# Optimization experiments

Hardware: AMD Instinct MI355X
Metric: run time of the kernel (lower is better)

The kernel has to match this reference:

```python
import jax, jax.numpy as jnp
import numpy as np

N_NODES = 50000   # batch_size * n_verts
N_EDGES = 800000
D_FEAT = 128
UNITS = 256


def setup_inputs() -> dict:
    key = jax.random.key(0)
    k1, k2, k3, k4, k5 = jax.random.split(key, 5)
    features = jax.random.normal(k1, (N_NODES, D_FEAT), dtype=jnp.float32)
    edge_row = jax.random.randint(k2, (N_EDGES,), 0, N_NODES, dtype=jnp.int32)
    edge_col = jax.random.randint(k3, (N_EDGES,), 0, N_NODES, dtype=jnp.int32)
    edge_val = jax.random.uniform(k4, (N_EDGES,), dtype=jnp.float32)
    W = jax.random.normal(k5, (D_FEAT, UNITS), dtype=jnp.float32) * (1.0 / np.sqrt(D_FEAT))
    return {"features": features, "edge_row": edge_row, "edge_col": edge_col,
            "edge_val": edge_val, "W": W}


def reference(features, edge_row, edge_col, edge_val, W):
    # features: [N, F] (already the (batch*n_verts, F) layout the layer reshapes to)
    # A in COO: A[edge_row[e], edge_col[e]] = edge_val[e]
    n = features.shape[0]
    # in_degree = row-sum of A values, +1 for self loop
    in_degree = jax.ops.segment_sum(edge_val, edge_row, num_segments=n) + 1.0
    invsqrt_deg = jax.lax.rsqrt(in_degree)                       # [N]
    normalized = invsqrt_deg[:, None] * features                 # [N, F]
    # pooled = A @ normalized  (gather source rows, scale, scatter-add to dest)
    msgs = edge_val[:, None] * normalized[edge_col]              # [E, F]
    pooled = jax.ops.segment_sum(msgs, edge_row, num_segments=n) # [N, F]
    # self-loop contribution (normalized case)
    pooled = pooled + invsqrt_deg[:, None] * normalized
    # dense projection + relu
    out = jax.nn.relu(pooled @ W)                                # [N, units]
    return out
```

## Files before the change

### kernel.cpp

```cpp
#include <hip/hip_runtime.h>

constexpr int N = 50000;
constexpr int E = 800000;
constexpr int F = 128;
constexpr int U = 256;

constexpr int R    = 4;
constexpr int NK   = N * R;
constexpr int EBLK = E / 256;
constexpr int SBLK = (NK + 255) / 256;

typedef __attribute__((ext_vector_type(8))) short short8;
typedef __attribute__((ext_vector_type(4))) float float4v;

constexpr float FIXED_SCALE = 67108864.0f;
constexpr float FIXED_INV   = 1.4901161193847656e-8f;
constexpr unsigned long long VAL_MASK = 0xFFFFFFFFFFull;

__device__ inline unsigned short f32_to_bf16(float x) {
    unsigned int u = __float_as_uint(x);
    unsigned int r = (u + 0x7fffu + ((u >> 16) & 1u)) >> 16;
    return (unsigned short)r;
}
__device__ inline float bf_lo(unsigned int u) { return __uint_as_float(u << 16); }
__device__ inline float bf_hi(unsigned int u) { return __uint_as_float(u & 0xffff0000u); }

__global__ __launch_bounds__(256) void hist_kernel(const int* __restrict__ erow,
                                                   const float* __restrict__ eval,
                                                   unsigned long long* __restrict__ packed,
                                                   unsigned int* __restrict__ rankp,
                                                   const float* __restrict__ W,
                                                   unsigned short* __restrict__ Wt) {
    if (blockIdx.x >= EBLK) {
        int idx = (blockIdx.x - EBLK) * 256 + threadIdx.x;
        int k = idx >> 8;
        int n = idx & 255;
        Wt[n * F + k] = f32_to_bf16(W[idx]);
        return;
    }
    int e = blockIdx.x * 256 + threadIdx.x;
    int key = erow[e] * R + (blockIdx.x & (R - 1));
    unsigned long long add =
        (1ull << 40) | (unsigned long long)(eval[e] * FIXED_SCALE);
    unsigned long long old = atomicAdd(&packed[key], add);
    rankp[e] = ((unsigned int)key << 12) | (unsigned int)(old >> 40);
}

__global__ __launch_bounds__(256) void blksum_kernel(const unsigned long long* __restrict__ packed,
                                                     int* __restrict__ blk_sum) {
    int i = blockIdx.x * 256 + threadIdx.x;
    int v = (i < NK) ? (int)(packed[i] >> 40) : 0;
    #pragma unroll
    for (int off = 32; off > 0; off >>= 1) v += __shfl_down(v, off, 64);
    __shared__ int s[4];
    if ((threadIdx.x & 63) == 0) s[threadIdx.x >> 6] = v;
    __syncthreads();
    if (threadIdx.x == 0) blk_sum[blockIdx.x] = s[0] + s[1] + s[2] + s[3];
}

__global__ __launch_bounds__(256) void blkscan_kernel(const unsigned long long* __restrict__ packed,
                                                      const int* __restrict__ blk_sum,
                                                      int* __restrict__ rp2) {
    __shared__ int sh[256];
    __shared__ int waves[4];
    __shared__ int base_sh;
    int t = threadIdx.x;
    int bid = blockIdx.x;

    int pre = 0;
    for (int idx = t; idx < bid; idx += 256) pre += blk_sum[idx];
    #pragma unroll
    for (int off = 32; off > 0; off >>= 1) pre += __shfl_down(pre, off, 64);
    if ((t & 63) == 0) waves[t >> 6] = pre;
    __syncthreads();
    if (t == 0) base_sh = waves[0] + waves[1] + waves[2] + waves[3];

    int i = bid * 256 + t;
    int v = (i < NK) ? (int)(packed[i] >> 40) : 0;
    sh[t] = v;
    __syncthreads();
    for (int off = 1; off < 256; off <<= 1) {
        int u = (t >= off) ? sh[t - off] : 0;
        __syncthreads();
        sh[t] += u;
        __syncthreads();
    }
    if (i < NK) rp2[i] = base_sh + sh[t] - v;
    if (bid == 0 && t == 0) rp2[NK] = E;
}

__global__ __launch_bounds__(256) void permute_kernel(const int* __restrict__ ecol,
                                                      const float* __restrict__ eval,
                                                      const unsigned int* __restrict__ rankp,
                                                      const int* __restrict__ rp2,
                                                      int2* __restrict__ csr) {
    int e = blockIdx.x * 256 + threadIdx.x;
    if (e < E) {
        unsigned int pk = rankp[e];
        int p = rp2[pk >> 12] + (int)(pk & 0xFFFu);
        csr[p] = make_int2(ecol[e], __float_as_int(eval[e]));
    }
}

__global__ __launch_bounds__(256) void norm_kernel(const float* __restrict__ feat,
                                                   const unsigned long long* __restrict__ packed,
                                                   float* __restrict__ iv,
                                                   unsigned int* __restrict__ nrm) {
    int gtid = blockIdx.x * 256 + threadIdx.x;
    int n    = gtid >> 6;
    int lane = threadIdx.x & 63;
    if (n >= N) return;

    int kb = n * R;
    unsigned long long s = (packed[kb] & VAL_MASK) + (packed[kb + 1] & VAL_MASK) +
                           (packed[kb + 2] & VAL_MASK) + (packed[kb + 3] & VAL_MASK);
    float iv_ = rsqrtf((float)s * FIXED_INV + 1.0f);
    if (lane == 0) iv[n] = iv_;

    float2 f = ((const float2*)feat)[n * 64 + lane];
    nrm[n * 64 + lane] =
        (unsigned int)f32_to_bf16(iv_ * f.x) | ((unsigned int)f32_to_bf16(iv_ * f.y) << 16);
}

__global__ __launch_bounds__(256) void gather_kernel(const int* __restrict__ rp2,
                                                     const int2* __restrict__ csr,
                                                     const unsigned int* __restrict__ nrm,
                                                     const float* __restrict__ iv,
                                                     unsigned int* __restrict__ pooledb) {
    int gtid = blockIdx.x * 256 + threadIdx.x;
    int n    = gtid >> 6;
    int lane = threadIdx.x & 63;
    if (n >= N) return;

    float iv_ = iv[n];
    unsigned int self = nrm[n * 64 + lane];
    float acc0 = iv_ * bf_lo(self);
    float acc1 = iv_ * bf_hi(self);

    int e = rp2[n * R], e1 = rp2[n * R + R];
    for (; e + 7 < e1; e += 8) {
        int2 p0 = csr[e],     p1 = csr[e + 1], p2 = csr[e + 2], p3 = csr[e + 3];
        int2 p4 = csr[e + 4], p5 = csr[e + 5], p6 = csr[e + 6], p7 = csr[e + 7];
        unsigned int u0 = nrm[(size_t)p0.x * 64 + lane];
        unsigned int u1 = nrm[(size_t)p1.x * 64 + lane];
        unsigned int u2 = nrm[(size_t)p2.x * 64 + lane];
        unsigned int u3 = nrm[(size_t)p3.x * 64 + lane];
        unsigned int u4 = nrm[(size_t)p4.x * 64 + lane];
        unsigned int u5 = nrm[(size_t)p5.x * 64 + lane];
        unsigned int u6 = nrm[(size_t)p6.x * 64 + lane];
        unsigned int u7 = nrm[(size_t)p7.x * 64 + lane];
        acc0 += __int_as_float(p0.y) * bf_lo(u0); acc1 += __int_as_float(p0.y) * bf_hi(u0);
        acc0 += __int_as_float(p1.y) * bf_lo(u1); acc1 += __int_as_float(p1.y) * bf_hi(u1);
        acc0 += __int_as_float(p2.y) * bf_lo(u2); acc1 += __int_as_float(p2.y) * bf_hi(u2);
        acc0 += __int_as_float(p3.y) * bf_lo(u3); acc1 += __int_as_float(p3.y) * bf_hi(u3);
        acc0 += __int_as_float(p4.y) * bf_lo(u4); acc1 += __int_as_float(p4.y) * bf_hi(u4);
        acc0 += __int_as_float(p5.y) * bf_lo(u5); acc1 += __int_as_float(p5.y) * bf_hi(u5);
        acc0 += __int_as_float(p6.y) * bf_lo(u6); acc1 += __int_as_float(p6.y) * bf_hi(u6);
        acc0 += __int_as_float(p7.y) * bf_lo(u7); acc1 += __int_as_float(p7.y) * bf_hi(u7);
    }
    for (; e + 3 < e1; e += 4) {
        int2 p0 = csr[e], p1 = csr[e + 1], p2 = csr[e + 2], p3 = csr[e + 3];
        unsigned int u0 = nrm[(size_t)p0.x * 64 + lane];
        unsigned int u1 = nrm[(size_t)p1.x * 64 + lane];
        unsigned int u2 = nrm[(size_t)p2.x * 64 + lane];
        unsigned int u3 = nrm[(size_t)p3.x * 64 + lane];
        acc0 += __int_as_float(p0.y) * bf_lo(u0); acc1 += __int_as_float(p0.y) * bf_hi(u0);
        acc0 += __int_as_float(p1.y) * bf_lo(u1); acc1 += __int_as_float(p1.y) * bf_hi(u1);
        acc0 += __int_as_float(p2.y) * bf_lo(u2); acc1 += __int_as_float(p2.y) * bf_hi(u2);
        acc0 += __int_as_float(p3.y) * bf_lo(u3); acc1 += __int_as_float(p3.y) * bf_hi(u3);
    }
    for (; e < e1; ++e) {
        int2 p0 = csr[e];
        unsigned int u0 = nrm[(size_t)p0.x * 64 + lane];
        acc0 += __int_as_float(p0.y) * bf_lo(u0);
        acc1 += __int_as_float(p0.y) * bf_hi(u0);
    }
    pooledb[n * 64 + lane] =
        (unsigned int)f32_to_bf16(acc0) | ((unsigned int)f32_to_bf16(acc1) << 16);
}

__global__ __launch_bounds__(256) void gemm_mfma_kernel(const unsigned short* __restrict__ Ab,
                                                        const unsigned short* __restrict__ Wt,
                                                        float* __restrict__ out) {
    __shared__ unsigned short As[16384];
    __shared__ unsigned short Bs[16384];
    const int tid = threadIdx.x;
    const int m0 = blockIdx.x * 128;
    const int n0 = blockIdx.y * 128;

    {
        const int r = tid >> 1;
        const int h = tid & 1;
        const int grow = m0 + r;
        const uint4* asrc = (grow < N) ? (const uint4*)(Ab + (size_t)grow * F) : nullptr;
        const uint4* bsrc = (const uint4*)(Wt + (size_t)(n0 + r) * F);
        #pragma unroll
        for (int j = 0; j < 8; ++j) {
            int o = h * 8 + j;
            int ks = o >> 2, quad = o & 3;
            int slot = ((ks * 8 + (r >> 4)) * 64) + (quad << 4) + (r & 15);
            uint4 av = asrc ? asrc[o] : make_uint4(0u, 0u, 0u, 0u);
            ((uint4*)As)[slot] = av;
            ((uint4*)Bs)[slot] = bsrc[o];
        }
    }
    __syncthreads();

    const int wave = tid >> 6;
    const int lane = tid & 63;
    float4v acc[8][2];
    #pragma unroll
    for (int i = 0; i < 8; ++i) {
        acc[i][0] = (float4v){0.f, 0.f, 0.f, 0.f};
        acc[i][1] = (float4v){0.f, 0.f, 0.f, 0.f};
    }

    #pragma unroll
    for (int ks = 0; ks < 4; ++ks) {
        short8 b0 = *(const short8*)&Bs[(((ks * 8 + wave * 2 + 0) * 64) + lane) * 8];
        short8 b1 = *(const short8*)&Bs[(((ks * 8 + wave * 2 + 1) * 64) + lane) * 8];
        #pragma unroll
        for (int mt = 0; mt < 8; ++mt) {
            short8 a = *(const short8*)&As[(((ks * 8 + mt) * 64) + lane) * 8];
            acc[mt][0] = __builtin_amdgcn_mfma_f32_16x16x32_bf16(a, b0, acc[mt][0], 0, 0, 0);
            acc[mt][1] = __builtin_amdgcn_mfma_f32_16x16x32_bf16(a, b1, acc[mt][1], 0, 0, 0);
        }
    }

    const int quad = lane >> 4;
    const int colt = lane & 15;
    #pragma unroll
    for (int mt = 0; mt < 8; ++mt) {
        #pragma unroll
        for (int nt = 0; nt < 2; ++nt) {
            int col = n0 + (wave * 2 + nt) * 16 + colt;
            #pragma unroll
            for (int i = 0; i < 4; ++i) {
                int row = m0 + mt * 16 + quad * 4 + i;
                if (row < N) out[(size_t)row * U + col] = fmaxf(acc[mt][nt][i], 0.f);
            }
        }
    }
}

extern "C" void kernel_launch(void* const* d_in, const int* in_sizes, int n_in,
                              void* d_out, int out_size, void* d_ws, size_t ws_size,
                              hipStream_t stream) {
    (void)in_sizes; (void)n_in; (void)out_size; (void)ws_size;

    const float* feat = (const float*)d_in[0];
    const int*   erow = (const int*)d_in[1];
    const int*   ecol = (const int*)d_in[2];
    const float* eval = (const float*)d_in[3];
    const float* W    = (const float*)d_in[4];
    float* out = (float*)d_out;

    char* ws = (char*)d_ws;
    unsigned long long* packed = (unsigned long long*)(ws + 0);
    int*            blk_sum = (int*)(ws + 1600000);
    int*            rp2     = (int*)(ws + 1603200);
    unsigned int*   rankp   = (unsigned int*)(ws + 2403264);
    int2*           csr     = (int2*)(ws + 5603264);
    float*          iv      = (float*)(ws + 12003264);
    unsigned short* Wt      = (unsigned short*)(ws + 12203264);
    unsigned int*   nrm     = (unsigned int*)(ws + 12268800);
    unsigned int*   pooledb = (unsigned int*)(ws + 25068800);

    (void)hipMemsetAsync(packed, 0, (size_t)NK * 8, stream);

    hist_kernel<<<EBLK + (F * U) / 256, 256, 0, stream>>>(erow, eval, packed, rankp, W, Wt);

    blksum_kernel<<<SBLK, 256, 0, stream>>>(packed, blk_sum);
    blkscan_kernel<<<SBLK, 256, 0, stream>>>(packed, blk_sum, rp2);

    permute_kernel<<<EBLK, 256, 0, stream>>>(ecol, eval, rankp, rp2, csr);
    norm_kernel  <<<(N * 64) / 256, 256, 0, stream>>>(feat, packed, iv, nrm);
    gather_kernel<<<(N * 64) / 256, 256, 0, stream>>>(rp2, csr, nrm, iv, pooledb);

    dim3 ggrid((N + 127) / 128, U / 128);
    gemm_mfma_kernel<<<ggrid, 256, 0, stream>>>((const unsigned short*)pooledb, Wt, out);
}
```

Measured before the change: 220.0 us.

## Fuse CSR-build front stages into one cooperative kernel with grid syncs

Replaces the memset, histogram, block-sum, block-scan, permute and normalize launches with a single cooperative kernel of 1024 blocks that uses grid-wide syncs between phases, with a multi-launch fallback. It also doubles the atomic spreading factor R from 4 to 8 to reduce atomic contention on row counters. The aim is to remove launch gaps and tail effects. In exchange, the scan pass now processes twice as many keys, the blkscan prefix loop over blk_sum grows, and grid syncs add their own cost.

```diff
diff --git a/kernel.cpp b/kernel.cpp
--- a/kernel.cpp
+++ b/kernel.cpp
@@ -1,11 +1,14 @@
 #include <hip/hip_runtime.h>
+#include <hip/hip_cooperative_groups.h>
+
+namespace cg = cooperative_groups;
 
 constexpr int N = 50000;
 constexpr int E = 800000;
 constexpr int F = 128;
 constexpr int U = 256;
 
-constexpr int R    = 4;
+constexpr int R    = 8;
 constexpr int NK   = N * R;
 constexpr int EBLK = E / 256;
 constexpr int SBLK = (NK + 255) / 256;
@@ -24,6 +27,121 @@
 }
 __device__ inline float bf_lo(unsigned int u) { return __uint_as_float(u << 16); }
 __device__ inline float bf_hi(unsigned int u) { return __uint_as_float(u & 0xffff0000u); }
+
+__device__ inline void p_zero(unsigned long long* packed, int g0, int gsz) {
+    for (int i = g0; i < NK; i += gsz) packed[i] = 0ull;
+}
+
+__device__ inline void p_hist(const int* erow, const float* eval,
+                              unsigned long long* packed, unsigned int* rankp,
+                              const float* W, unsigned short* Wt, int g0, int gsz) {
+    for (int e = g0; e < E; e += gsz) {
+        int key = erow[e] * R + ((e >> 8) & (R - 1));
+        unsigned long long add =
+            (1ull << 40) | (unsigned long long)(eval[e] * FIXED_SCALE);
+        unsigned long long old = atomicAdd(&packed[key], add);
+        rankp[e] = ((unsigned int)key << 12) | (unsigned int)(old >> 40);
+    }
+    for (int idx = g0; idx < F * U; idx += gsz) {
+        int k = idx >> 8, n = idx & 255;
+        Wt[n * F + k] = f32_to_bf16(W[idx]);
+    }
+}
+
+__device__ inline void p_blksum(const unsigned long long* packed, int* blk_sum,
+                                int bid0, int bstride, int t) {
+    __shared__ int s4[4];
+    for (int c = bid0; c < SBLK; c += bstride) {
+        int i = c * 256 + t;
+        int v = (i < NK) ? (int)(packed[i] >> 40) : 0;
+        #pragma unroll
+        for (int off = 32; off > 0; off >>= 1) v += __shfl_down(v, off, 64);
+        if ((t & 63) == 0) s4[t >> 6] = v;
+        __syncthreads();
+        if (t == 0) blk_sum[c] = s4[0] + s4[1] + s4[2] + s4[3];
+        __syncthreads();
+    }
+}
+
+__device__ inline void p_blkscan(const unsigned long long* packed, const int* blk_sum,
+                                 int* rp2, int bid0, int bstride, int t, int g0) {
+    __shared__ int sh[256];
+    __shared__ int waves[4];
+    __shared__ int base_sh;
+    for (int c = bid0; c < SBLK; c += bstride) {
+        int pre = 0;
+        for (int idx = t; idx < c; idx += 256) pre += blk_sum[idx];
+        #pragma unroll
+        for (int off = 32; off > 0; off >>= 1) pre += __shfl_down(pre, off, 64);
+        if ((t & 63) == 0) waves[t >> 6] = pre;
+        __syncthreads();
+        if (t == 0) base_sh = waves[0] + waves[1] + waves[2] + waves[3];
+        int i = c * 256 + t;
+        int v = (i < NK) ? (int)(packed[i] >> 40) : 0;
+        sh[t] = v;
+        __syncthreads();
+        for (int off = 1; off < 256; off <<= 1) {
+            int u = (t >= off) ? sh[t - off] : 0;
+            __syncthreads();
+            sh[t] += u;
+            __syncthreads();
+        }
+        if (i < NK) rp2[i] = base_sh + sh[t] - v;
+        __syncthreads();
+    }
+    if (g0 == 0) rp2[NK] = E;
+}
+
+__device__ inline void p_permute_norm(const int* ecol, const float* eval,
+                                      const unsigned int* rankp, const int* rp2,
+                                      int2* csr, const unsigned long long* packed,
+                                      const float* feat, float* iv, unsigned int* nrm,
+                                      int g0, int gsz, int t) {
+    for (int e = g0; e < E; e += gsz) {
+        unsigned int pk = rankp[e];
+        int p = rp2[pk >> 12] + (int)(pk & 0xFFFu);
+        csr[p] = make_int2(ecol[e], __float_as_int(eval[e]));
+    }
+    int lane = t & 63;
+    int w0 = g0 >> 6;
+    int wstride = gsz >> 6;
+    for (int n = w0; n < N; n += wstride) {
+        int kb = n * R;
+        unsigned long long s = 0;
+        #pragma unroll
+        for (int j = 0; j < R; ++j) s += packed[kb + j] & VAL_MASK;
+        float iv_ = rsqrtf((float)s * FIXED_INV + 1.0f);
+        if (lane == 0) iv[n] = iv_;
+        float2 f = ((const float2*)feat)[n * 64 + lane];
+        nrm[n * 64 + lane] =
+            (unsigned int)f32_to_bf16(iv_ * f.x) | ((unsigned int)f32_to_bf16(iv_ * f.y) << 16);
+    }
+}
+
+__global__ __launch_bounds__(256) void fused_front_kernel(
+    const int* __restrict__ erow, const float* __restrict__ eval,
+    const int* __restrict__ ecol, const float* __restrict__ W,
+    const float* __restrict__ feat,
+    unsigned long long* __restrict__ packed, unsigned int* __restrict__ rankp,
+    int* __restrict__ blk_sum, int* __restrict__ rp2,
+    int2* __restrict__ csr, float* __restrict__ iv,
+    unsigned short* __restrict__ Wt, unsigned int* __restrict__ nrm) {
+    cg::grid_group grid = cg::this_grid();
+    const int nb  = gridDim.x;
+    const int gsz = nb * 256;
+    const int t   = threadIdx.x;
+    const int g0  = blockIdx.x * 256 + t;
+
+    p_zero(packed, g0, gsz);
+    grid.sync();
+    p_hist(erow, eval, packed, rankp, W, Wt, g0, gsz);
+    grid.sync();
+    p_blksum(packed, blk_sum, blockIdx.x, nb, t);
+    grid.sync();
+    p_blkscan(packed, blk_sum, rp2, blockIdx.x, nb, t, g0);
+    grid.sync();
+    p_permute_norm(ecol, eval, rankp, rp2, csr, packed, feat, iv, nrm, g0, gsz, t);
+}
 
 __global__ __launch_bounds__(256) void hist_kernel(const int* __restrict__ erow,
                                                    const float* __restrict__ eval,
@@ -31,95 +149,30 @@
                                                    unsigned int* __restrict__ rankp,
                                                    const float* __restrict__ W,
                                                    unsigned short* __restrict__ Wt) {
-    if (blockIdx.x >= EBLK) {
-        int idx = (blockIdx.x - EBLK) * 256 + threadIdx.x;
-        int k = idx >> 8;
-        int n = idx & 255;
-        Wt[n * F + k] = f32_to_bf16(W[idx]);
-        return;
-    }
-    int e = blockIdx.x * 256 + threadIdx.x;
-    int key = erow[e] * R + (blockIdx.x & (R - 1));
-    unsigned long long add =
-        (1ull << 40) | (unsigned long long)(eval[e] * FIXED_SCALE);
-    unsigned long long old = atomicAdd(&packed[key], add);
-    rankp[e] = ((unsigned int)key << 12) | (unsigned int)(old >> 40);
-}
-
+    p_hist(erow, eval, packed, rankp, W, Wt,
+           blockIdx.x * 256 + threadIdx.x, gridDim.x * 256);
+}
 __global__ __launch_bounds__(256) void blksum_kernel(const unsigned long long* __restrict__ packed,
                                                      int* __restrict__ blk_sum) {
-    int i = blockIdx.x * 256 + threadIdx.x;
-    int v = (i < NK) ? (int)(packed[i] >> 40) : 0;
-    #pragma unroll
-    for (int off = 32; off > 0; off >>= 1) v += __shfl_down(v, off, 64);
-    __shared__ int s[4];
-    if ((threadIdx.x & 63) == 0) s[threadIdx.x >> 6] = v;
-    __syncthreads();
-    if (threadIdx.x == 0) blk_sum[blockIdx.x] = s[0] + s[1] + s[2] + s[3];
-}
-
+    p_blksum(packed, blk_sum, blockIdx.x, gridDim.x, threadIdx.x);
+}
 __global__ __launch_bounds__(256) void blkscan_kernel(const unsigned long long* __restrict__ packed,
                                                       const int* __restrict__ blk_sum,
                                                       int* __restrict__ rp2) {
-    __shared__ int sh[256];
-    __shared__ int waves[4];
-    __shared__ int base_sh;
-    int t = threadIdx.x;
-    int bid = blockIdx.x;
-
-    int pre = 0;
-    for (int idx = t; idx < bid; idx += 256) pre += blk_sum[idx];
-    #pragma unroll
-    for (int off = 32; off > 0; off >>= 1) pre += __shfl_down(pre, off, 64);
-    if ((t & 63) == 0) waves[t >> 6] = pre;
-    __syncthreads();
-    if (t == 0) base_sh = waves[0] + waves[1] + waves[2] + waves[3];
-
-    int i = bid * 256 + t;
-    int v = (i < NK) ? (int)(packed[i] >> 40) : 0;
-    sh[t] = v;
-    __syncthreads();
-    for (int off = 1; off < 256; off <<= 1) {
-        int u = (t >= off) ? sh[t - off] : 0;
-        __syncthreads();
-        sh[t] += u;
-        __syncthreads();
-    }
-    if (i < NK) rp2[i] = base_sh + sh[t] - v;
-    if (bid == 0 && t == 0) rp2[NK] = E;
-}
-
-__global__ __launch_bounds__(256) void permute_kernel(const int* __restrict__ ecol,
-                                                      const float* __restrict__ eval,
-                                                      const unsigned int* __restrict__ rankp,
-                                                      const int* __restrict__ rp2,
-                                                      int2* __restrict__ csr) {
-    int e = blockIdx.x * 256 + threadIdx.x;
-    if (e < E) {
-        unsigned int pk = rankp[e];
-        int p = rp2[pk >> 12] + (int)(pk & 0xFFFu);
-        csr[p] = make_int2(ecol[e], __float_as_int(eval[e]));
-    }
-}
-
-__global__ __launch_bounds__(256) void norm_kernel(const float* __restrict__ feat,
-                                                   const unsigned long long* __restrict__ packed,
-                                                   float* __restrict__ iv,
-                                                   unsigned int* __restrict__ nrm) {
-    int gtid = blockIdx.x * 256 + threadIdx.x;
-    int n    = gtid >> 6;
-    int lane = threadIdx.x & 63;
-    if (n >= N) return;
-
-    int kb = n * R;
-    unsigned long long s = (packed[kb] & VAL_MASK) + (packed[kb + 1] & VAL_MASK) +
-                           (packed[kb + 2] & VAL_MASK) + (packed[kb + 3] & VAL_MASK);
-    float iv_ = rsqrtf((float)s * FIXED_INV + 1.0f);
-    if (lane == 0) iv[n] = iv_;
-
-    float2 f = ((const float2*)feat)[n * 64 + lane];
-    nrm[n * 64 + lane] =
-        (unsigned int)f32_to_bf16(iv_ * f.x) | ((unsigned int)f32_to_bf16(iv_ * f.y) << 16);
+    p_blkscan(packed, blk_sum, rp2, blockIdx.x, gridDim.x, threadIdx.x,
+              blockIdx.x * 256 + threadIdx.x);
+}
+__global__ __launch_bounds__(256) void pn_kernel(const int* __restrict__ ecol,
+                                                 const float* __restrict__ eval,
+                                                 const unsigned int* __restrict__ rankp,
+                                                 const int* __restrict__ rp2,
+                                                 int2* __restrict__ csr,
+                                                 const unsigned long long* __restrict__ packed,
+                                                 const float* __restrict__ feat,
+                                                 float* __restrict__ iv,
+                                                 unsigned int* __restrict__ nrm) {
+    p_permute_norm(ecol, eval, rankp, rp2, csr, packed, feat, iv, nrm,
+                   blockIdx.x * 256 + threadIdx.x, gridDim.x * 256, threadIdx.x);
 }
 
 __global__ __launch_bounds__(256) void gather_kernel(const int* __restrict__ rp2,
@@ -257,24 +310,28 @@
 
     char* ws = (char*)d_ws;
     unsigned long long* packed = (unsigned long long*)(ws + 0);
-    int*            blk_sum = (int*)(ws + 1600000);
-    int*            rp2     = (int*)(ws + 1603200);
-    unsigned int*   rankp   = (unsigned int*)(ws + 2403264);
-    int2*           csr     = (int2*)(ws + 5603264);
-    float*          iv      = (float*)(ws + 12003264);
-    unsigned short* Wt      = (unsigned short*)(ws + 12203264);
-    unsigned int*   nrm     = (unsigned int*)(ws + 12268800);
-    unsigned int*   pooledb = (unsigned int*)(ws + 25068800);
-
-    (void)hipMemsetAsync(packed, 0, (size_t)NK * 8, stream);
-
-    hist_kernel<<<EBLK + (F * U) / 256, 256, 0, stream>>>(erow, eval, packed, rankp, W, Wt);
-
-    blksum_kernel<<<SBLK, 256, 0, stream>>>(packed, blk_sum);
-    blkscan_kernel<<<SBLK, 256, 0, stream>>>(packed, blk_sum, rp2);
-
-    permute_kernel<<<EBLK, 256, 0, stream>>>(ecol, eval, rankp, rp2, csr);
-    norm_kernel  <<<(N * 64) / 256, 256, 0, stream>>>(feat, packed, iv, nrm);
+    int*            blk_sum = (int*)(ws + 3200000);
+    int*            rp2     = (int*)(ws + 3206400);
+    unsigned int*   rankp   = (unsigned int*)(ws + 4806464);
+    int2*           csr     = (int2*)(ws + 8006464);
+    float*          iv      = (float*)(ws + 14406464);
+    unsigned short* Wt      = (unsigned short*)(ws + 14606464);
+    unsigned int*   nrm     = (unsigned int*)(ws + 14672000);
+    unsigned int*   pooledb = (unsigned int*)(ws + 27472000);
+
+    void* kargs[] = {(void*)&erow, (void*)&eval, (void*)&ecol, (void*)&W, (void*)&feat,
+                     (void*)&packed, (void*)&rankp, (void*)&blk_sum, (void*)&rp2,
+                     (void*)&csr, (void*)&iv, (void*)&Wt, (void*)&nrm};
+    hipError_t cerr = hipLaunchCooperativeKernel((void*)fused_front_kernel,
+                                                 dim3(1024), dim3(256), kargs, 0, stream);
+    if (cerr != hipSuccess) {
+        (void)hipMemsetAsync(packed, 0, (size_t)NK * 8, stream);
+        hist_kernel<<<EBLK, 256, 0, stream>>>(erow, eval, packed, rankp, W, Wt);
+        blksum_kernel<<<SBLK, 256, 0, stream>>>(packed, blk_sum);
+        blkscan_kernel<<<SBLK, 256, 0, stream>>>(packed, blk_sum, rp2);
+        pn_kernel<<<EBLK, 256, 0, stream>>>(ecol, eval, rankp, rp2, csr, packed, feat, iv, nrm);
+    }
+
     gather_kernel<<<(N * 64) / 256, 256, 0, stream>>>(rp2, csr, nrm, iv, pooledb);
 
     dim3 ggrid((N + 127) / 128, U / 128);
```

New measurement: 603.2 us. 2.74x slower.
